# Kernel tuning notes

Hardware: AMD Instinct MI355X
Metric: run time of the kernel (lower is better)

## Reference

```python
import jax, jax.numpy as jnp
import numpy as np

D_MODEL = 1024
H = 16
HEAD = D_MODEL // H  # 64


def setup_inputs() -> dict:
    key = jax.random.key(0)
    ks = jax.random.split(key, 10)
    B, S = 2, 2048
    x = jax.random.normal(ks[0], (B, S, D_MODEL), dtype=jnp.float32)
    y = jax.random.normal(ks[1], (B, S, D_MODEL), dtype=jnp.float32)
    mask = jnp.ones((B, S, S), dtype=jnp.float32)
    s = 1.0 / np.sqrt(D_MODEL)
    Wq = jax.random.normal(ks[2], (D_MODEL, D_MODEL), dtype=jnp.float32) * s
    Wk = jax.random.normal(ks[3], (D_MODEL, D_MODEL), dtype=jnp.float32) * s
    Wv = jax.random.normal(ks[4], (D_MODEL, D_MODEL), dtype=jnp.float32) * s
    Wo = jax.random.normal(ks[5], (D_MODEL, D_MODEL), dtype=jnp.float32) * s
    bq = jnp.zeros((D_MODEL,), jnp.float32)
    bk = jnp.zeros((D_MODEL,), jnp.float32)
    bv = jnp.zeros((D_MODEL,), jnp.float32)
    bo = jnp.zeros((D_MODEL,), jnp.float32)
    return {"x": x, "y": y, "mask": mask, "Wq": Wq, "bq": bq, "Wk": Wk,
            "bk": bk, "Wv": Wv, "bv": bv, "Wo": Wo, "bo": bo}


def reference(x, y, mask, Wq, bq, Wk, bk, Wv, bv, Wo, bo):
    # torch Linear: out = in @ W.T + b; here W stored as [out, in]
    B, Sq, D = x.shape
    Skv = y.shape[1]
    q = x @ Wq.T + bq  # [B, Sq, D]
    k = y @ Wk.T + bk  # [B, Skv, D]
    v = y @ Wv.T + bv
    # chunk(h, dim=-1) + cat(dim=0) == split feature dim into heads (head-major)
    q = q.reshape(B, Sq, H, HEAD)
    k = k.reshape(B, Skv, H, HEAD)
    v = v.reshape(B, Skv, H, HEAD)
    score = jnp.einsum('bqhd,bkhd->bhqk', q, k) / np.sqrt(HEAD)
    score = score + (1.0 - mask[:, None, :, :]) * -1e9
    attn = jax.nn.softmax(score, axis=-1)
    out = jnp.einsum('bhqk,bkhd->bqhd', attn, v).reshape(B, Sq, D)
    return out @ Wo.T + bo
```

## Files before the change

kernel.cpp:

```cpp
#include <hip/hip_runtime.h>
#include <cstdint>
#include <cstddef>

typedef __bf16 bf16x8 __attribute__((ext_vector_type(8)));
typedef float f32x4 __attribute__((ext_vector_type(4)));
typedef unsigned short u16;
typedef unsigned short u16x8 __attribute__((ext_vector_type(8)));
typedef unsigned int u32;

typedef __attribute__((address_space(1))) void gvoid_t;
typedef __attribute__((address_space(3))) void lvoid_t;

__device__ __forceinline__ void gld_lds16(const void* g, void* l) {
  __builtin_amdgcn_global_load_lds((gvoid_t*)g, (lvoid_t*)l, 16, 0, 0);
}

__device__ __forceinline__ u16 f2bf(float f) {
  u32 u = __float_as_uint(f);
  u += 0x7fffu + ((u >> 16) & 1u);
  return (u16)(u >> 16);
}
__device__ __forceinline__ u32 pack_rnd(float a, float b) {
  const u32 ua = __float_as_uint(a) + 0x8000u;
  const u32 ub = __float_as_uint(b) + 0x8000u;
  return __builtin_amdgcn_perm(ub, ua, 0x07060302u);
}
__device__ __forceinline__ bf16x8 ld_frag(const u16* p) {
  return __builtin_bit_cast(bf16x8, *(const uint4*)p);
}
__device__ __forceinline__ f32x4 mfma16(bf16x8 a, bf16x8 b, f32x4 c) {
  return __builtin_amdgcn_mfma_f32_16x16x32_bf16(a, b, c, 0, 0, 0);
}
__device__ __forceinline__ float ex2(float x) {
  return __builtin_amdgcn_exp2f(x);
}

#define D_MODEL 1024
#define SEQ     2048
#define NHEAD   16
#define QSC     0.1803368801f
#define MBIAS   (-1.4426950408e9f)

__global__ __launch_bounds__(256) void pre_kernel(
    const float* __restrict__ x,  const float* __restrict__ y,
    const float* __restrict__ wq, const float* __restrict__ wk,
    const float* __restrict__ wv, const float* __restrict__ wo,
    const float* __restrict__ mask,
    u16* __restrict__ xb, u16* __restrict__ yb,
    u16* __restrict__ wqb, u16* __restrict__ wkb,
    u16* __restrict__ wvb, u16* __restrict__ wob,
    u16* __restrict__ biasC) {
  const int bid = blockIdx.x;
  const float* src;
  u16* dst;
  int base;
  float sA = 1.0f, sB = 0.0f;
  if (bid < 2048)      { src = x;    dst = xb;    base = 0; }
  else if (bid < 4096) { src = y;    dst = yb;    base = 2048; }
  else if (bid < 4608) { src = wq;   dst = wqb;   base = 4096; sA = QSC; }
  else if (bid < 5120) { src = wk;   dst = wkb;   base = 4608; }
  else if (bid < 5632) { src = wv;   dst = wvb;   base = 5120; }
  else if (bid < 6144) { src = wo;   dst = wob;   base = 5632; }
  else                 { src = mask; dst = biasC; base = 6144; sA = -MBIAS; sB = MBIAS; }
  const int i = (((bid - base) * 256) + threadIdx.x) * 8;
  const float4 a = *(const float4*)(src + i);
  const float4 b = *(const float4*)(src + i + 4);
  ushort4 lo, hi;
  lo.x = f2bf(a.x * sA + sB); lo.y = f2bf(a.y * sA + sB);
  lo.z = f2bf(a.z * sA + sB); lo.w = f2bf(a.w * sA + sB);
  hi.x = f2bf(b.x * sA + sB); hi.y = f2bf(b.y * sA + sB);
  hi.z = f2bf(b.z * sA + sB); hi.w = f2bf(b.w * sA + sB);
  *(ushort4*)(dst + i) = lo;
  *(ushort4*)(dst + i + 4) = hi;
}

template <int MODE, typename OT>
__device__ __forceinline__ void gemm_block_128(const u16* __restrict__ A,
                                               const u16* __restrict__ W,
                                               const float* __restrict__ bias,
                                               float bscale,
                                               OT* __restrict__ D,
                                               int mb, int nb) {
  __shared__ __align__(16) u16 S[16384];
  u16* Asl = S;
  u16* Bsl = S + 8192;
  const int tid = threadIdx.x;
  const int w = tid >> 6, lane = tid & 63, quad = lane >> 4, l16 = lane & 15;
  const int wm = (w & 1) * 64, wn = (w >> 1) * 64;
  const int cidx = w * 64 + lane;

  f32x4 acc[4][4];
#pragma unroll
  for (int i = 0; i < 4; ++i)
#pragma unroll
    for (int j = 0; j < 4; ++j) acc[i][j] = f32x4{0.f, 0.f, 0.f, 0.f};

  for (int k0 = 0; k0 < 1024; k0 += 64) {
    __syncthreads();
#pragma unroll
    for (int t = 0; t < 4; ++t) {
      const int idx = t * 256 + cidx;
      const int row = idx >> 3;
      const int g = (idx & 7) ^ (row & 7);
      const size_t dst = (size_t)(t * 4 + w) * 1024;
      gld_lds16(A + (size_t)(mb * 128 + row) * 1024 + k0 + g * 8, (char*)Asl + dst);
      gld_lds16(W + (size_t)(nb * 128 + row) * 1024 + k0 + g * 8, (char*)Bsl + dst);
    }
    __syncthreads();

#pragma unroll
    for (int kk = 0; kk < 2; ++kk) {
      bf16x8 af[4], bfr[4];
#pragma unroll
      for (int i = 0; i < 4; ++i) {
        const int ar = wm + i * 16 + l16;
        const int br = wn + i * 16 + l16;
        af[i]  = ld_frag(Asl + ar * 64 + (((kk * 4 + quad) ^ (ar & 7)) * 8));
        bfr[i] = ld_frag(Bsl + br * 64 + (((kk * 4 + quad) ^ (br & 7)) * 8));
      }
#pragma unroll
      for (int i = 0; i < 4; ++i)
#pragma unroll
        for (int j = 0; j < 4; ++j) acc[i][j] = mfma16(af[i], bfr[j], acc[i][j]);
    }
  }

  if constexpr (MODE == 2) {
    __syncthreads();
#pragma unroll
    for (int i = 0; i < 4; ++i)
#pragma unroll
      for (int j = 0; j < 4; ++j) {
        const int dl = wn + j * 16 + l16;
        const float bv = bias[nb * 128 + dl];
        const int sx = (wm + i * 16 + quad * 4) ^ ((dl & 15) << 3);
        uint2 pv;
        pv.x = (u32)f2bf(acc[i][j][0] + bv) | ((u32)f2bf(acc[i][j][1] + bv) << 16);
        pv.y = (u32)f2bf(acc[i][j][2] + bv) | ((u32)f2bf(acc[i][j][3] + bv) << 16);
        *(uint2*)(S + dl * 128 + sx) = pv;
      }
    __syncthreads();
    const int dl = tid >> 1, half = tid & 1;
    const int bb = mb >> 4, s0 = (mb & 15) * 128;
    u16* vrow = (u16*)D + (size_t)(bb * 1024 + nb * 128 + dl) * SEQ + s0 + half * 64;
#pragma unroll
    for (int c = 0; c < 8; ++c) {
      const int pc = (half * 8 + c) ^ (dl & 15);
      *(uint4*)(vrow + c * 8) = *(const uint4*)(S + dl * 128 + pc * 8);
    }
  } else {
#pragma unroll
    for (int i = 0; i < 4; ++i)
#pragma unroll
      for (int j = 0; j < 4; ++j) {
        const int gn = nb * 128 + wn + j * 16 + l16;
        const float bv = bias[gn] * bscale;
#pragma unroll
        for (int r = 0; r < 4; ++r) {
          const int gm = mb * 128 + wm + i * 16 + quad * 4 + r;
          const float v = acc[i][j][r] + bv;
          if constexpr (sizeof(OT) == 2)
            D[(size_t)gm * 1024 + gn] = (OT)f2bf(v);
          else
            D[(size_t)gm * 1024 + gn] = (OT)v;
        }
      }
  }
}

__global__ __launch_bounds__(256) void qkv_kernel(
    const u16* __restrict__ xb, const u16* __restrict__ yb,
    const u16* __restrict__ Wqb, const u16* __restrict__ Wkb, const u16* __restrict__ Wvb,
    const float* __restrict__ bq, const float* __restrict__ bk, const float* __restrict__ bv,
    u16* __restrict__ qb, u16* __restrict__ kb, u16* __restrict__ vt) {
  const int mat = blockIdx.y >> 3;
  const int nb = blockIdx.y & 7;
  const int mb = blockIdx.x;
  if (mat == 0)      gemm_block_128<0, u16>(xb, Wqb, bq, QSC,  qb, mb, nb);
  else if (mat == 1) gemm_block_128<0, u16>(yb, Wkb, bk, 1.0f, kb, mb, nb);
  else               gemm_block_128<2, u16>(yb, Wvb, bv, 1.0f, vt, mb, nb);
}

__global__ __launch_bounds__(256) void oproj_kernel(
    const u16* __restrict__ ctx, const u16* __restrict__ Wob,
    const float* __restrict__ bo, float* __restrict__ out) {
  gemm_block_128<1, float>(ctx, Wob, bo, 1.0f, out, blockIdx.x, blockIdx.y);
}

__global__ __launch_bounds__(256) void attn_kernel(
    const u16* __restrict__ qb, const u16* __restrict__ kb,
    const u16* __restrict__ vt, const u16* __restrict__ biasC,
    u16* __restrict__ ctx) {
  const int h = blockIdx.x;
  const int qblk = blockIdx.y;
  const int b = blockIdx.z;
  const int tid = threadIdx.x, w = tid >> 6, lane = tid & 63;
  const int quad = lane >> 4, l16 = lane & 15;
  const int q0 = qblk * 64;

  __shared__ __align__(16) u16 Ks[64 * 64];
  __shared__ __align__(16) u16 Vs[64 * 64];
  __shared__ __align__(16) u16 BP[64 * 64];

  const int qrow = w * 16 + l16;
  const u16* qp = qb + (size_t)(b * SEQ + q0 + qrow) * D_MODEL + h * 64;
  const bf16x8 qf0 = ld_frag(qp + quad * 8);
  const bf16x8 qf1 = ld_frag(qp + 32 + quad * 8);

  bf16x8 onesf;
  {
    u16x8 t;
    const u16 ov = (l16 == 0) ? (u16)0x3F80 : (u16)0;
#pragma unroll
    for (int j = 0; j < 8; ++j) t[j] = ov;
    onesf = __builtin_bit_cast(bf16x8, t);
  }

  f32x4 O[4];
#pragma unroll
  for (int dt = 0; dt < 4; ++dt) O[dt] = f32x4{0.f, 0.f, 0.f, 0.f};
  f32x4 O4 = f32x4{0.f, 0.f, 0.f, 0.f};

  const int cidx = w * 64 + lane;
  const int bhalf = (quad & 1) * 4;

  const int r0 = cidx >> 3,        g0 = (cidx & 7) ^ (r0 & 7);
  const int r1 = (256 + cidx) >> 3, g1 = ((256 + cidx) & 7) ^ (r1 & 7);
  const u16* kp0 = kb + (size_t)(b * SEQ + r0) * D_MODEL + h * 64 + g0 * 8;
  const u16* kp1 = kb + (size_t)(b * SEQ + r1) * D_MODEL + h * 64 + g1 * 8;
  const u16* vp0 = vt + ((size_t)((b * NHEAD + h) * 64 + r0)) * SEQ + g0 * 8;
  const u16* vp1 = vt + ((size_t)((b * NHEAD + h) * 64 + r1)) * SEQ + g1 * 8;
  const u16* bp0 = biasC + (size_t)(b * SEQ + q0 + r0) * SEQ + g0 * 8;
  const u16* bp1 = biasC + (size_t)(b * SEQ + q0 + r1) * SEQ + g1 * 8;
  char* ld0 = (char*)nullptr;
  const size_t dst0 = (size_t)w * 1024;
  const size_t dst1 = (size_t)(4 + w) * 1024;
  (void)ld0;

  for (int kt = 0; kt < 32; ++kt) {
    __syncthreads();
    gld_lds16(kp0, (char*)Ks + dst0);
    gld_lds16(kp1, (char*)Ks + dst1);
    gld_lds16(vp0, (char*)Vs + dst0);
    gld_lds16(vp1, (char*)Vs + dst1);
    gld_lds16(bp0, (char*)BP + dst0);
    gld_lds16(bp1, (char*)BP + dst1);
    kp0 += 64 * D_MODEL; kp1 += 64 * D_MODEL;
    vp0 += 64;           vp1 += 64;
    bp0 += 64;           bp1 += 64;
    __syncthreads();

    f32x4 z[4];
#pragma unroll
    for (int nt = 0; nt < 4; ++nt) {
      const int kvl = nt * 16 + l16;
      const bf16x8 kf0 = ld_frag(Ks + kvl * 64 + ((quad ^ (kvl & 7)) * 8));
      const bf16x8 kf1 = ld_frag(Ks + kvl * 64 + (((4 + quad) ^ (kvl & 7)) * 8));
      const int ck = nt * 2 + (quad >> 1);
      const uint2 bw = *(const uint2*)(BP + qrow * 64 + ((ck ^ (qrow & 7)) * 8) + bhalf);
      f32x4 zz;
      zz[0] = __uint_as_float(bw.x << 16);
      zz[1] = __uint_as_float(bw.x & 0xffff0000u);
      zz[2] = __uint_as_float(bw.y << 16);
      zz[3] = __uint_as_float(bw.y & 0xffff0000u);
      zz = mfma16(kf0, qf0, zz);
      zz = mfma16(kf1, qf1, zz);
      z[nt] = zz;
    }
#pragma unroll
    for (int nt = 0; nt < 4; ++nt) {
      uint2 pv;
      pv.x = pack_rnd(ex2(z[nt][0]), ex2(z[nt][1]));
      pv.y = pack_rnd(ex2(z[nt][2]), ex2(z[nt][3]));
      const int ck = nt * 2 + (quad >> 1);
      *(uint2*)(BP + qrow * 64 + ((ck ^ (qrow & 7)) * 8) + bhalf) = pv;
    }

    const bf16x8 pf0 = ld_frag(BP + qrow * 64 + ((quad ^ (qrow & 7)) * 8));
    const bf16x8 pf1 = ld_frag(BP + qrow * 64 + (((4 + quad) ^ (qrow & 7)) * 8));
#pragma unroll
    for (int dt = 0; dt < 4; ++dt) {
      const int vr = dt * 16 + l16;
      const bf16x8 vf0 = ld_frag(Vs + vr * 64 + ((quad ^ (vr & 7)) * 8));
      const bf16x8 vf1 = ld_frag(Vs + vr * 64 + (((4 + quad) ^ (vr & 7)) * 8));
      O[dt] = mfma16(pf0, vf0, O[dt]);
      O[dt] = mfma16(pf1, vf1, O[dt]);
    }
    O4 = mfma16(pf0, onesf, O4);
    O4 = mfma16(pf1, onesf, O4);
  }

  float inv[4];
#pragma unroll
  for (int r = 0; r < 4; ++r)
    inv[r] = 1.0f / __shfl(O4[r], lane & 48, 64);

#pragma unroll
  for (int dt = 0; dt < 4; ++dt)
#pragma unroll
    for (int r = 0; r < 4; ++r) {
      const int gq = b * SEQ + q0 + w * 16 + quad * 4 + r;
      const int gd = h * 64 + dt * 16 + l16;
      ctx[(size_t)gq * D_MODEL + gd] = f2bf(O[dt][r] * inv[r]);
    }
}

extern "C" void kernel_launch(void* const* d_in, const int* in_sizes, int n_in,
                              void* d_out, int out_size, void* d_ws, size_t ws_size,
                              hipStream_t stream) {
  (void)in_sizes; (void)n_in; (void)out_size; (void)ws_size;
  const float* x    = (const float*)d_in[0];
  const float* y    = (const float*)d_in[1];
  const float* mask = (const float*)d_in[2];
  const float* Wq   = (const float*)d_in[3];
  const float* bq   = (const float*)d_in[4];
  const float* Wk   = (const float*)d_in[5];
  const float* bk   = (const float*)d_in[6];
  const float* Wv   = (const float*)d_in[7];
  const float* bv   = (const float*)d_in[8];
  const float* Wo   = (const float*)d_in[9];
  const float* bo   = (const float*)d_in[10];
  float* out = (float*)d_out;

  const size_t M4 = (size_t)4096 * 1024;
  const size_t M1 = (size_t)1024 * 1024;
  u16* qbuf  = (u16*)d_ws;
  u16* kbuf  = qbuf + M4;
  u16* vt    = kbuf + M4;
  u16* cbuf  = vt + M4;
  u16* wob   = cbuf + M4;
  u16* xb    = wob + M1;
  u16* yb    = xb + M4;
  u16* wqb   = yb + M4;
  u16* wkb   = wqb + M1;
  u16* wvb   = wkb + M1;
  u16* biasC = (u16*)d_out;

  pre_kernel<<<dim3(10240, 1, 1), 256, 0, stream>>>(
      x, y, Wq, Wk, Wv, Wo, mask, xb, yb, wqb, wkb, wvb, wob, biasC);
  qkv_kernel<<<dim3(32, 24, 1), 256, 0, stream>>>(xb, yb, wqb, wkb, wvb,
                                                  bq, bk, bv, qbuf, kbuf, vt);
  attn_kernel<<<dim3(NHEAD, 32, 2), 256, 0, stream>>>(qbuf, kbuf, vt, biasC, cbuf);
  oproj_kernel<<<dim3(32, 8, 1), 256, 0, stream>>>(cbuf, wob, bo, out);
}
```

Measured before the change: 261.3 us.

## Double-buffer K/V/bias LDS tiles in attention with prefetch and setprio

The attention kernel now keeps two LDS buffers each for K, V and the bias/P tile. It issues the global-to-LDS loads for the next KV block before computing on the current one, and drops to a single barrier per iteration. This is meant to hide global load latency behind the QK^T, exp and PV MFMA work. It also raises wave priority around the MFMA sections. In exchange, LDS per block doubles to about 48KB, which can lower how many blocks fit on a CU.

New measurement: 282.7 us. 1.08x slower.

```diff
diff --git a/kernel.cpp b/kernel.cpp
--- a/kernel.cpp
+++ b/kernel.cpp
@@ -198,9 +198,9 @@
   const int quad = lane >> 4, l16 = lane & 15;
   const int q0 = qblk * 64;
 
-  __shared__ __align__(16) u16 Ks[64 * 64];
-  __shared__ __align__(16) u16 Vs[64 * 64];
-  __shared__ __align__(16) u16 BP[64 * 64];
+  __shared__ __align__(16) u16 Ks[2][64 * 64];
+  __shared__ __align__(16) u16 Vs[2][64 * 64];
+  __shared__ __align__(16) u16 BP[2][64 * 64];
 
   const int qrow = w * 16 + l16;
   const u16* qp = qb + (size_t)(b * SEQ + q0 + qrow) * D_MODEL + h * 64;
@@ -232,32 +232,49 @@
   const u16* vp1 = vt + ((size_t)((b * NHEAD + h) * 64 + r1)) * SEQ + g1 * 8;
   const u16* bp0 = biasC + (size_t)(b * SEQ + q0 + r0) * SEQ + g0 * 8;
   const u16* bp1 = biasC + (size_t)(b * SEQ + q0 + r1) * SEQ + g1 * 8;
-  char* ld0 = (char*)nullptr;
   const size_t dst0 = (size_t)w * 1024;
   const size_t dst1 = (size_t)(4 + w) * 1024;
-  (void)ld0;
+
+  gld_lds16(kp0, (char*)Ks[0] + dst0);
+  gld_lds16(kp1, (char*)Ks[0] + dst1);
+  gld_lds16(vp0, (char*)Vs[0] + dst0);
+  gld_lds16(vp1, (char*)Vs[0] + dst1);
+  gld_lds16(bp0, (char*)BP[0] + dst0);
+  gld_lds16(bp1, (char*)BP[0] + dst1);
+  kp0 += 64 * D_MODEL; kp1 += 64 * D_MODEL;
+  vp0 += 64;           vp1 += 64;
+  bp0 += 64;           bp1 += 64;
+  __syncthreads();
 
   for (int kt = 0; kt < 32; ++kt) {
-    __syncthreads();
-    gld_lds16(kp0, (char*)Ks + dst0);
-    gld_lds16(kp1, (char*)Ks + dst1);
-    gld_lds16(vp0, (char*)Vs + dst0);
-    gld_lds16(vp1, (char*)Vs + dst1);
-    gld_lds16(bp0, (char*)BP + dst0);
-    gld_lds16(bp1, (char*)BP + dst1);
-    kp0 += 64 * D_MODEL; kp1 += 64 * D_MODEL;
-    vp0 += 64;           vp1 += 64;
-    bp0 += 64;           bp1 += 64;
-    __syncthreads();
+    const int cur = kt & 1;
+    if (kt < 31) {
+      char* kD = (char*)Ks[cur ^ 1];
+      char* vD = (char*)Vs[cur ^ 1];
+      char* bD = (char*)BP[cur ^ 1];
+      gld_lds16(kp0, kD + dst0);
+      gld_lds16(kp1, kD + dst1);
+      gld_lds16(vp0, vD + dst0);
+      gld_lds16(vp1, vD + dst1);
+      gld_lds16(bp0, bD + dst0);
+      gld_lds16(bp1, bD + dst1);
+      kp0 += 64 * D_MODEL; kp1 += 64 * D_MODEL;
+      vp0 += 64;           vp1 += 64;
+      bp0 += 64;           bp1 += 64;
+    }
+    const u16* Kc = Ks[cur];
+    const u16* Vc = Vs[cur];
+    u16* Bc = BP[cur];
 
     f32x4 z[4];
+    __builtin_amdgcn_s_setprio(1);
 #pragma unroll
     for (int nt = 0; nt < 4; ++nt) {
       const int kvl = nt * 16 + l16;
-      const bf16x8 kf0 = ld_frag(Ks + kvl * 64 + ((quad ^ (kvl & 7)) * 8));
-      const bf16x8 kf1 = ld_frag(Ks + kvl * 64 + (((4 + quad) ^ (kvl & 7)) * 8));
+      const bf16x8 kf0 = ld_frag(Kc + kvl * 64 + ((quad ^ (kvl & 7)) * 8));
+      const bf16x8 kf1 = ld_frag(Kc + kvl * 64 + (((4 + quad) ^ (kvl & 7)) * 8));
       const int ck = nt * 2 + (quad >> 1);
-      const uint2 bw = *(const uint2*)(BP + qrow * 64 + ((ck ^ (qrow & 7)) * 8) + bhalf);
+      const uint2 bw = *(const uint2*)(Bc + qrow * 64 + ((ck ^ (qrow & 7)) * 8) + bhalf);
       f32x4 zz;
       zz[0] = __uint_as_float(bw.x << 16);
       zz[1] = __uint_as_float(bw.x & 0xffff0000u);
@@ -267,27 +284,32 @@
       zz = mfma16(kf1, qf1, zz);
       z[nt] = zz;
     }
+    __builtin_amdgcn_s_setprio(0);
 #pragma unroll
     for (int nt = 0; nt < 4; ++nt) {
       uint2 pv;
       pv.x = pack_rnd(ex2(z[nt][0]), ex2(z[nt][1]));
       pv.y = pack_rnd(ex2(z[nt][2]), ex2(z[nt][3]));
       const int ck = nt * 2 + (quad >> 1);
-      *(uint2*)(BP + qrow * 64 + ((ck ^ (qrow & 7)) * 8) + bhalf) = pv;
-    }
-
-    const bf16x8 pf0 = ld_frag(BP + qrow * 64 + ((quad ^ (qrow & 7)) * 8));
-    const bf16x8 pf1 = ld_frag(BP + qrow * 64 + (((4 + quad) ^ (qrow & 7)) * 8));
+      *(uint2*)(Bc + qrow * 64 + ((ck ^ (qrow & 7)) * 8) + bhalf) = pv;
+    }
+
+    const bf16x8 pf0 = ld_frag(Bc + qrow * 64 + ((quad ^ (qrow & 7)) * 8));
+    const bf16x8 pf1 = ld_frag(Bc + qrow * 64 + (((4 + quad) ^ (qrow & 7)) * 8));
+    __builtin_amdgcn_s_setprio(1);
 #pragma unroll
     for (int dt = 0; dt < 4; ++dt) {
       const int vr = dt * 16 + l16;
-      const bf16x8 vf0 = ld_frag(Vs + vr * 64 + ((quad ^ (vr & 7)) * 8));
-      const bf16x8 vf1 = ld_frag(Vs + vr * 64 + (((4 + quad) ^ (vr & 7)) * 8));
+      const bf16x8 vf0 = ld_frag(Vc + vr * 64 + ((quad ^ (vr & 7)) * 8));
+      const bf16x8 vf1 = ld_frag(Vc + vr * 64 + (((4 + quad) ^ (vr & 7)) * 8));
       O[dt] = mfma16(pf0, vf0, O[dt]);
       O[dt] = mfma16(pf1, vf1, O[dt]);
     }
     O4 = mfma16(pf0, onesf, O4);
     O4 = mfma16(pf1, onesf, O4);
+    __builtin_amdgcn_s_setprio(0);
+
+    __syncthreads();
   }
 
   float inv[4];
```

## Skip bias tile loads for fully unmasked attention blocks via per-tile flags

Applied to the files above, without the earlier changes.

The mask conversion pass now records, per 64x64 query/key tile, whether any mask entry differs from one, using wave ballots and atomicOr into a small flags array. The attention kernel reads these flags and skips loading and adding the bias tile when the tile is fully unmasked, which cuts global-to-LDS traffic. It also raises wave priority around the MFMA sections. This adds a memset and atomics in the preprocessing pass and a per-iteration branch in attention.

After: 250.5 us. -4.1%, faster.

```diff
diff --git a/kernel.cpp b/kernel.cpp
--- a/kernel.cpp
+++ b/kernel.cpp
@@ -49,7 +49,7 @@
     u16* __restrict__ xb, u16* __restrict__ yb,
     u16* __restrict__ wqb, u16* __restrict__ wkb,
     u16* __restrict__ wvb, u16* __restrict__ wob,
-    u16* __restrict__ biasC) {
+    u16* __restrict__ biasC, u32* __restrict__ flags) {
   const int bid = blockIdx.x;
   const float* src;
   u16* dst;
@@ -72,6 +72,24 @@
   hi.z = f2bf(b.z * sA + sB); hi.w = f2bf(b.w * sA + sB);
   *(ushort4*)(dst + i) = lo;
   *(ushort4*)(dst + i + 4) = hi;
+
+  if (bid >= 6144) {
+    const bool m8 = (a.x != 1.f) || (a.y != 1.f) || (a.z != 1.f) || (a.w != 1.f) ||
+                    (b.x != 1.f) || (b.y != 1.f) || (b.z != 1.f) || (b.w != 1.f);
+    const unsigned long long bal = __ballot(m8);
+    const int lane = threadIdx.x & 63, wv8 = threadIdx.x >> 6;
+    if (lane == 0) {
+      u32 bits = 0;
+#pragma unroll
+      for (int g = 0; g < 8; ++g)
+        bits |= (((bal >> (8 * g)) & 0xFFull) ? 1u : 0u) << g;
+      if (bits) {
+        const int row = bid - 6144;
+        const int bb = row >> 11, q = row & 2047;
+        atomicOr(&flags[bb * 32 + (q >> 6)], bits << (wv8 * 8));
+      }
+    }
+  }
 }
 
 template <int MODE, typename OT>
@@ -190,7 +208,7 @@
 __global__ __launch_bounds__(256) void attn_kernel(
     const u16* __restrict__ qb, const u16* __restrict__ kb,
     const u16* __restrict__ vt, const u16* __restrict__ biasC,
-    u16* __restrict__ ctx) {
+    const u32* __restrict__ flags, u16* __restrict__ ctx) {
   const int h = blockIdx.x;
   const int qblk = blockIdx.y;
   const int b = blockIdx.z;
@@ -201,6 +219,8 @@
   __shared__ __align__(16) u16 Ks[64 * 64];
   __shared__ __align__(16) u16 Vs[64 * 64];
   __shared__ __align__(16) u16 BP[64 * 64];
+
+  const u32 fl = flags[(b << 5) + qblk];
 
   const int qrow = w * 16 + l16;
   const u16* qp = qb + (size_t)(b * SEQ + q0 + qrow) * D_MODEL + h * 64;
@@ -232,41 +252,48 @@
   const u16* vp1 = vt + ((size_t)((b * NHEAD + h) * 64 + r1)) * SEQ + g1 * 8;
   const u16* bp0 = biasC + (size_t)(b * SEQ + q0 + r0) * SEQ + g0 * 8;
   const u16* bp1 = biasC + (size_t)(b * SEQ + q0 + r1) * SEQ + g1 * 8;
-  char* ld0 = (char*)nullptr;
   const size_t dst0 = (size_t)w * 1024;
   const size_t dst1 = (size_t)(4 + w) * 1024;
-  (void)ld0;
 
   for (int kt = 0; kt < 32; ++kt) {
+    const bool doBias = (fl >> kt) & 1u;
     __syncthreads();
     gld_lds16(kp0, (char*)Ks + dst0);
     gld_lds16(kp1, (char*)Ks + dst1);
     gld_lds16(vp0, (char*)Vs + dst0);
     gld_lds16(vp1, (char*)Vs + dst1);
-    gld_lds16(bp0, (char*)BP + dst0);
-    gld_lds16(bp1, (char*)BP + dst1);
+    if (doBias) {
+      gld_lds16(bp0, (char*)BP + dst0);
+      gld_lds16(bp1, (char*)BP + dst1);
+    }
     kp0 += 64 * D_MODEL; kp1 += 64 * D_MODEL;
     vp0 += 64;           vp1 += 64;
     bp0 += 64;           bp1 += 64;
     __syncthreads();
 
     f32x4 z[4];
+    __builtin_amdgcn_s_setprio(1);
 #pragma unroll
     for (int nt = 0; nt < 4; ++nt) {
       const int kvl = nt * 16 + l16;
       const bf16x8 kf0 = ld_frag(Ks + kvl * 64 + ((quad ^ (kvl & 7)) * 8));
       const bf16x8 kf1 = ld_frag(Ks + kvl * 64 + (((4 + quad) ^ (kvl & 7)) * 8));
-      const int ck = nt * 2 + (quad >> 1);
-      const uint2 bw = *(const uint2*)(BP + qrow * 64 + ((ck ^ (qrow & 7)) * 8) + bhalf);
       f32x4 zz;
-      zz[0] = __uint_as_float(bw.x << 16);
-      zz[1] = __uint_as_float(bw.x & 0xffff0000u);
-      zz[2] = __uint_as_float(bw.y << 16);
-      zz[3] = __uint_as_float(bw.y & 0xffff0000u);
+      if (doBias) {
+        const int ck = nt * 2 + (quad >> 1);
+        const uint2 bw = *(const uint2*)(BP + qrow * 64 + ((ck ^ (qrow & 7)) * 8) + bhalf);
+        zz[0] = __uint_as_float(bw.x << 16);
+        zz[1] = __uint_as_float(bw.x & 0xffff0000u);
+        zz[2] = __uint_as_float(bw.y << 16);
+        zz[3] = __uint_as_float(bw.y & 0xffff0000u);
+      } else {
+        zz = f32x4{0.f, 0.f, 0.f, 0.f};
+      }
       zz = mfma16(kf0, qf0, zz);
       zz = mfma16(kf1, qf1, zz);
       z[nt] = zz;
     }
+    __builtin_amdgcn_s_setprio(0);
 #pragma unroll
     for (int nt = 0; nt < 4; ++nt) {
       uint2 pv;
@@ -278,6 +305,7 @@
 
     const bf16x8 pf0 = ld_frag(BP + qrow * 64 + ((quad ^ (qrow & 7)) * 8));
     const bf16x8 pf1 = ld_frag(BP + qrow * 64 + (((4 + quad) ^ (qrow & 7)) * 8));
+    __builtin_amdgcn_s_setprio(1);
 #pragma unroll
     for (int dt = 0; dt < 4; ++dt) {
       const int vr = dt * 16 + l16;
@@ -288,6 +316,7 @@
     }
     O4 = mfma16(pf0, onesf, O4);
     O4 = mfma16(pf1, onesf, O4);
+    __builtin_amdgcn_s_setprio(0);
   }
 
   float inv[4];
@@ -334,12 +363,14 @@
   u16* wqb   = yb + M4;
   u16* wkb   = wqb + M1;
   u16* wvb   = wkb + M1;
+  u32* flags = (u32*)(wvb + M1);
   u16* biasC = (u16*)d_out;
 
+  hipMemsetAsync(flags, 0, 64 * sizeof(u32), stream);
   pre_kernel<<<dim3(10240, 1, 1), 256, 0, stream>>>(
-      x, y, Wq, Wk, Wv, Wo, mask, xb, yb, wqb, wkb, wvb, wob, biasC);
+      x, y, Wq, Wk, Wv, Wo, mask, xb, yb, wqb, wkb, wvb, wob, biasC, flags);
   qkv_kernel<<<dim3(32, 24, 1), 256, 0, stream>>>(xb, yb, wqb, wkb, wvb,
                                                   bq, bk, bv, qbuf, kbuf, vt);
-  attn_kernel<<<dim3(NHEAD, 32, 2), 256, 0, stream>>>(qbuf, kbuf, vt, biasC, cbuf);
+  attn_kernel<<<dim3(NHEAD, 32, 2), 256, 0, stream>>>(qbuf, kbuf, vt, biasC, flags, cbuf);
   oproj_kernel<<<dim3(32, 8, 1), 256, 0, stream>>>(cbuf, wob, bo, out);
 }
```
